# Optimization experiments

Hardware: AMD Instinct MI355X
Metric: run time of the kernel (lower is better)

The kernel has to match this reference:

```python
import jax, jax.numpy as jnp
import numpy as np

NUM_HEADS = 32
NUM_KV_HEADS = 8
HEAD_DIM = 128
SCALE = 0.08838834764831845  # 1/sqrt(HEAD_DIM)
SEQ_LEN = 2048
NEG_INF = -1e30


def setup_inputs() -> dict:
    key = jax.random.key(0)
    k1, k2, k3 = jax.random.split(key, 3)
    query = jax.random.normal(k1, (SEQ_LEN, NUM_HEADS * HEAD_DIM), dtype=jnp.float32)
    key_t = jax.random.normal(k2, (SEQ_LEN, NUM_KV_HEADS * HEAD_DIM), dtype=jnp.float32)
    value = jax.random.normal(k3, (SEQ_LEN, NUM_KV_HEADS * HEAD_DIM), dtype=jnp.float32)
    return {"query": query, "key": key_t, "value": value}


def reference(query, key, value):
    S = query.shape[0]
    n_rep = NUM_HEADS // NUM_KV_HEADS
    # GQA: group q heads by kv head instead of materializing repeated K/V.
    q = query.reshape(S, NUM_KV_HEADS, n_rep, HEAD_DIM)   # [S, G, R, D]
    k = key.reshape(S, NUM_KV_HEADS, HEAD_DIM)            # [S, G, D]
    v = value.reshape(S, NUM_KV_HEADS, HEAD_DIM)          # [S, G, D]
    # scores: [G, R, S(query), S(key)]
    scores = jnp.einsum('sgrd,tgd->grst', q, k) * jnp.float32(SCALE)
    # causal mask (prefill: seq_len > 1 -> is_causal=True)
    causal = jnp.arange(S)[:, None] >= jnp.arange(S)[None, :]  # [S, S]
    scores = jnp.where(causal, scores, NEG_INF)
    probs = jax.nn.softmax(scores, axis=-1)
    out = jnp.einsum('grst,tgd->sgrd', probs, v)          # [S, G, R, D]
    return out.reshape(S, NUM_HEADS * HEAD_DIM)
```

## Files before the change

### kernel.cpp

```cpp
#include <hip/hip_runtime.h>


#define SEQ    2048
#define NH     32
#define NKV    8
#define DHEAD  128
#define QROW   (NH * DHEAD)
#define KVROW  (NKV * DHEAD)
#define SCALE  0.08838834764831845f
#define LOG2E  1.4426950408889634f
#define BN     64
#define PSTR   136

typedef __attribute__((ext_vector_type(8))) short bf16x8;
typedef __attribute__((ext_vector_type(8))) unsigned short u16x8;
typedef __attribute__((ext_vector_type(16))) float f32x16;
typedef __attribute__((ext_vector_type(4))) unsigned int u32x4;

static __device__ __forceinline__ unsigned short f2bf(float f) {
  unsigned int u = __float_as_uint(f);
  return (unsigned short)((u + 0x7fffu + ((u >> 16) & 1u)) >> 16);
}

static __device__ __forceinline__ unsigned cvtpk_bf16(float lo, float hi) {
  unsigned r;
  asm("v_cvt_pk_bf16_f32 %0, %1, %2" : "=v"(r) : "v"(lo), "v"(hi));
  return r;
}

static __device__ __forceinline__ f32x16 zero16() {
  f32x16 z;
#pragma unroll
  for (int i = 0; i < 16; ++i) z[i] = 0.f;
  return z;
}

__global__ __launch_bounds__(256) void prep_frag_kernel(
    const float* __restrict__ K, const float* __restrict__ V,
    unsigned short* __restrict__ Kf, unsigned short* __restrict__ Vf) {
  __shared__ unsigned short Ks[64 * PSTR];
  __shared__ unsigned short Vs[64 * PSTR];
  const int tb  = blockIdx.x;
  const int g   = blockIdx.y;
  const int t0  = tb * 64;
  const int tid = threadIdx.x;
#pragma unroll
  for (int e = 0; e < 8; ++e) {
    int fi = e * 256 + tid;
    int r  = fi >> 5;
    int c4 = fi & 31;
    const float4 kv = *(const float4*)(K + (size_t)(t0 + r) * KVROW + g * DHEAD + c4 * 4);
    ushort4 kb4 = {f2bf(kv.x), f2bf(kv.y), f2bf(kv.z), f2bf(kv.w)};
    *(ushort4*)&Ks[r * PSTR + c4 * 4] = kb4;
    const float4 vv = *(const float4*)(V + (size_t)(t0 + r) * KVROW + g * DHEAD + c4 * 4);
    ushort4 vb4 = {f2bf(vv.x), f2bf(vv.y), f2bf(vv.z), f2bf(vv.w)};
    *(ushort4*)&Vs[r * PSTR + c4 * 4] = vb4;
  }
  __syncthreads();
  const size_t tbase = ((size_t)(g * 32 + tb)) << 13;
#pragma unroll
  for (int q = 0; q < 4; ++q) {
    int slot = tid * 4 + q;
    int fk   = slot >> 6;
    int lane = slot & 63;
    int l32v = lane & 31, hiv = lane >> 5;
    int row  = (fk >> 3) * 32 + l32v;
    int col  = (fk & 7) * 16 + hiv * 8;
    u16x8 o = *(const u16x8*)&Ks[row * PSTR + col];
    *(u16x8*)(Kf + tbase + slot * 8) = o;
  }
#pragma unroll
  for (int q = 0; q < 4; ++q) {
    int slot = tid * 4 + q;
    int fv   = slot >> 6;
    int lane = slot & 63;
    int l32v = lane & 31, hiv = lane >> 5;
    int d    = (fv & 3) * 32 + l32v;
    int key  = (fv >> 2) * 16 + hiv * 8;
    u16x8 o;
#pragma unroll
    for (int j = 0; j < 8; ++j) o[j] = Vs[(key + j) * PSTR + d];
    *(u16x8*)(Vf + tbase + slot * 8) = o;
  }
}

static __device__ __forceinline__ void load_qf(
    const float* __restrict__ Q, int q0, int h, int l32, int hi, bf16x8* qf) {
  const float* qp = Q + (size_t)(q0 + l32) * QROW + h * DHEAD + hi * 8;
#pragma unroll
  for (int ks = 0; ks < 8; ++ks) {
    const float4 a = *(const float4*)(qp + ks * 16);
    const float4 c = *(const float4*)(qp + ks * 16 + 4);
    bf16x8 v;
    v[0] = (short)f2bf(a.x * (SCALE * LOG2E));
    v[1] = (short)f2bf(a.y * (SCALE * LOG2E));
    v[2] = (short)f2bf(a.z * (SCALE * LOG2E));
    v[3] = (short)f2bf(a.w * (SCALE * LOG2E));
    v[4] = (short)f2bf(c.x * (SCALE * LOG2E));
    v[5] = (short)f2bf(c.y * (SCALE * LOG2E));
    v[6] = (short)f2bf(c.z * (SCALE * LOG2E));
    v[7] = (short)f2bf(c.w * (SCALE * LOG2E));
    qf[ks] = v;
  }
}

#define PV_KSTEP(PP, S, KS2)                                                     \
  do {                                                                           \
    unsigned y0 = cvtpk_bf16((PP)[(2 * (S)) * 4 + 0], (PP)[(2 * (S)) * 4 + 1]);  \
    unsigned z0 = cvtpk_bf16((PP)[(2 * (S)) * 4 + 2], (PP)[(2 * (S)) * 4 + 3]);  \
    unsigned y1 = cvtpk_bf16((PP)[(2 * (S) + 1) * 4 + 0], (PP)[(2 * (S) + 1) * 4 + 1]); \
    unsigned z1 = cvtpk_bf16((PP)[(2 * (S) + 1) * 4 + 2], (PP)[(2 * (S) + 1) * 4 + 3]); \
    asm("v_permlane32_swap_b32 %0, %1" : "+v"(y0), "+v"(y1));                    \
    asm("v_permlane32_swap_b32 %0, %1" : "+v"(z0), "+v"(z1));                    \
    u32x4 paw = (u32x4){y0, z0, y1, z1};                                         \
    bf16x8 pa = __builtin_bit_cast(bf16x8, paw);                                 \
    _Pragma("unroll")                                                            \
    for (int nd = 0; nd < 4; ++nd) {                                             \
      bf16x8 vf = *(const bf16x8*)(Vt + ((KS2) * 4 + nd) * 512 + lane * 8);      \
      oacc[nd] = __builtin_amdgcn_mfma_f32_32x32x16_bf16(pa, vf, oacc[nd], 0, 0, 0); \
    }                                                                            \
  } while (0)

static __device__ __forceinline__ void compute_tile_g(
    const unsigned short* __restrict__ Kt, const unsigned short* __restrict__ Vt,
    const bf16x8* qf, f32x16* oacc, float& lsum,
    int keyb, int q0, bool diag, int KB, int l32, int hi, int lane) {
  bf16x8 kf[8], kf2[8];
#pragma unroll
  for (int ks = 0; ks < 8; ++ks)
    kf[ks] = *(const bf16x8*)(Kt + ks * 512 + lane * 8);
  if (KB == 2) {
#pragma unroll
    for (int ks = 0; ks < 8; ++ks)
      kf2[ks] = *(const bf16x8*)(Kt + (8 + ks) * 512 + lane * 8);
  }
  f32x16 s0 = zero16();
  f32x16 s1 = zero16();
  __builtin_amdgcn_s_setprio(1);
#pragma unroll
  for (int ks = 0; ks < 8; ++ks)
    s0 = __builtin_amdgcn_mfma_f32_32x32x16_bf16(kf[ks], qf[ks], s0, 0, 0, 0);
  if (KB == 2) {
#pragma unroll
    for (int ks = 0; ks < 8; ++ks)
      s1 = __builtin_amdgcn_mfma_f32_32x32x16_bf16(kf2[ks], qf[ks], s1, 0, 0, 0);
  }
  __builtin_amdgcn_s_setprio(0);

  f32x16 p0, p1;
  if (!diag) {
#pragma unroll
    for (int r = 0; r < 16; ++r) { float e = __builtin_amdgcn_exp2f(s0[r]); p0[r] = e; lsum += e; }
#pragma unroll
    for (int r = 0; r < 16; ++r) { float e = __builtin_amdgcn_exp2f(s1[r]); p1[r] = e; lsum += e; }
  } else {
#pragma unroll
    for (int r = 0; r < 16; ++r) {
      const int ko = (r & 3) + 8 * (r >> 2) + 4 * hi;
      float x = (keyb + ko > q0 + l32) ? -1e30f : s0[r];
      float e = __builtin_amdgcn_exp2f(x);
      p0[r] = e; lsum += e;
    }
    if (KB == 2) {
#pragma unroll
      for (int r = 0; r < 16; ++r) {
        const int ko = 32 + (r & 3) + 8 * (r >> 2) + 4 * hi;
        float x = (keyb + ko > q0 + l32) ? -1e30f : s1[r];
        float e = __builtin_amdgcn_exp2f(x);
        p1[r] = e; lsum += e;
      }
    }
  }

  __builtin_amdgcn_s_setprio(1);
  PV_KSTEP(p0, 0, 0);
  PV_KSTEP(p0, 1, 1);
  if (KB == 2) {
    PV_KSTEP(p1, 0, 2);
    PV_KSTEP(p1, 1, 3);
  }
  __builtin_amdgcn_s_setprio(0);
}

__global__ __launch_bounds__(512, 2) void sdpa_frag_kernel(
    const float* __restrict__ Q, float* __restrict__ O,
    const unsigned short* __restrict__ Kf, const unsigned short* __restrict__ Vf) {
  __shared__ float Obuf[4][32 * 128];
  __shared__ float Lb[4][32];

  const int b    = blockIdx.x;
  const int g    = b & 7;
  const int p    = b >> 3;
  const int nt_l = (p + 2) >> 1;
  const int nt_h = 33 - nt_l;
  const int jj_h = 63 - p;
  const int jj_l = p;
  const int tid  = threadIdx.x;
  const int w    = tid >> 6;
  const int lane = tid & 63;
  const int l32  = lane & 31;
  const int hi   = lane >> 5;
  const int grp  = w >> 2;
  const int wg   = w & 3;
  const int h    = g * 4 + wg;

  int q0 = (grp ? jj_l : jj_h) * 32;

  bf16x8 qf[8];
  load_qf(Q, q0, h, l32, hi, qf);

  f32x16 oacc[4];
#pragma unroll
  for (int i = 0; i < 4; ++i) oacc[i] = zero16();
  float lsum = 0.f;

  const int niters = grp ? 16 : 17;
#pragma unroll 1
  for (int i = 0; i < niters; ++i) {
    int t, jjc;
    bool diag;
    if (grp == 0)      { t = i;                jjc = jj_h; diag = (nt_h == 17) && (i == 16); }
    else if (i < nt_l) { t = i;                jjc = jj_l; diag = (i == nt_l - 1); }
    else               { t = 17 + i - nt_l;    jjc = jj_h; diag = (i == 15); }
    const int KB = (diag && !(jjc & 1)) ? 1 : 2;
    const unsigned short* Kt = Kf + (((size_t)(g * 32 + t)) << 13);
    const unsigned short* Vt = Vf + (((size_t)(g * 32 + t)) << 13);
    compute_tile_g(Kt, Vt, qf, oacc, lsum, t * BN, q0, diag, KB, l32, hi, lane);

    if (grp == 1 && i == nt_l - 1) {
      float tot = lsum + __shfl_xor(lsum, 32);
      float inv = 1.f / tot;
#pragma unroll
      for (int nd = 0; nd < 4; ++nd)
#pragma unroll
        for (int r = 0; r < 16; ++r) {
          const int row = (r & 3) + 8 * (r >> 2) + 4 * hi;
          O[(size_t)(q0 + row) * QROW + h * DHEAD + nd * 32 + l32] =
              oacc[nd][r] * __shfl(inv, row);
        }
#pragma unroll
      for (int i2 = 0; i2 < 4; ++i2) oacc[i2] = zero16();
      lsum = 0.f;
      q0 = jj_h * 32;
      load_qf(Q, q0, h, l32, hi, qf);
    }
  }

  float tot = lsum + __shfl_xor(lsum, 32);
  if (grp == 1) {
    if (hi == 0) Lb[wg][l32] = tot;
    float* ob = &Obuf[wg][0];
#pragma unroll
    for (int nd = 0; nd < 4; ++nd)
#pragma unroll
      for (int r = 0; r < 16; ++r) {
        const int row = (r & 3) + 8 * (r >> 2) + 4 * hi;
        ob[row * 128 + nd * 32 + l32] = oacc[nd][r];
      }
  }
  __syncthreads();
  if (grp == 0) {
    tot += Lb[wg][l32];
    float inv = 1.f / tot;
    const float* ob = &Obuf[wg][0];
#pragma unroll
    for (int nd = 0; nd < 4; ++nd)
#pragma unroll
      for (int r = 0; r < 16; ++r) {
        const int row = (r & 3) + 8 * (r >> 2) + 4 * hi;
        float val = oacc[nd][r] + ob[row * 128 + nd * 32 + l32];
        O[(size_t)(q0 + row) * QROW + h * DHEAD + nd * 32 + l32] =
            val * __shfl(inv, row);
      }
  }
}

extern "C" void kernel_launch(void* const* d_in, const int* in_sizes, int n_in,
                              void* d_out, int out_size, void* d_ws, size_t ws_size,
                              hipStream_t stream) {
  (void)in_sizes; (void)n_in; (void)out_size; (void)ws_size;
  const float* Q = (const float*)d_in[0];
  const float* K = (const float*)d_in[1];
  const float* V = (const float*)d_in[2];
  float* O = (float*)d_out;
  unsigned short* Kf = (unsigned short*)d_ws;
  unsigned short* Vf = Kf + (size_t)NKV * SEQ * DHEAD;
  prep_frag_kernel<<<dim3(32, 8), 256, 0, stream>>>(K, V, Kf, Vf);
  sdpa_frag_kernel<<<256, 512, 0, stream>>>(Q, O, Kf, Vf);
}
```

Before: 152.6 us.

## Split each query tile's key range across four waves with LDS atomic reduction

Replaces the paired light/heavy query-tile scheme, where 8 waves in a block cover 4 heads across two query tiles, with one block per (kv group, head, query tile). The four waves in that block stride over the causal key tiles and combine partial outputs and row sums through shared-memory atomics before a vectorized normalized store. The grid grows from 256 to 2048 blocks to balance load through scheduling rather than manual pairing. The setprio hints are also removed. In exchange, K/V tiles are no longer shared across the 4 heads within a block, and the LDS atomic reduction adds cost.

```diff
diff --git a/kernel.cpp b/kernel.cpp
--- a/kernel.cpp
+++ b/kernel.cpp
@@ -136,7 +136,6 @@
   }
   f32x16 s0 = zero16();
   f32x16 s1 = zero16();
-  __builtin_amdgcn_s_setprio(1);
 #pragma unroll
   for (int ks = 0; ks < 8; ++ks)
     s0 = __builtin_amdgcn_mfma_f32_32x32x16_bf16(kf[ks], qf[ks], s0, 0, 0, 0);
@@ -145,7 +144,6 @@
     for (int ks = 0; ks < 8; ++ks)
       s1 = __builtin_amdgcn_mfma_f32_32x32x16_bf16(kf2[ks], qf[ks], s1, 0, 0, 0);
   }
-  __builtin_amdgcn_s_setprio(0);
 
   f32x16 p0, p1;
   if (!diag) {
@@ -172,39 +170,33 @@
     }
   }
 
-  __builtin_amdgcn_s_setprio(1);
   PV_KSTEP(p0, 0, 0);
   PV_KSTEP(p0, 1, 1);
   if (KB == 2) {
     PV_KSTEP(p1, 0, 2);
     PV_KSTEP(p1, 1, 3);
   }
-  __builtin_amdgcn_s_setprio(0);
-}
-
-__global__ __launch_bounds__(512, 2) void sdpa_frag_kernel(
+}
+
+__global__ __launch_bounds__(256, 4) void sdpa_split4_kernel(
     const float* __restrict__ Q, float* __restrict__ O,
     const unsigned short* __restrict__ Kf, const unsigned short* __restrict__ Vf) {
-  __shared__ float Obuf[4][32 * 128];
-  __shared__ float Lb[4][32];
-
-  const int b    = blockIdx.x;
-  const int g    = b & 7;
-  const int p    = b >> 3;
-  const int nt_l = (p + 2) >> 1;
-  const int nt_h = 33 - nt_l;
-  const int jj_h = 63 - p;
-  const int jj_l = p;
+  __shared__ float Obuf[32 * 128];
+  __shared__ float Lbuf[32];
+
+  const int b      = blockIdx.x;
+  const int g      = b & 7;
+  const int hh     = (b >> 3) & 3;
+  const int jjcode = b >> 5;
+  const int jj     = 63 - jjcode;
+  const int q0     = jj * 32;
+  const int nt     = (jj >> 1) + 1;
   const int tid  = threadIdx.x;
-  const int w    = tid >> 6;
+  const int s    = tid >> 6;
   const int lane = tid & 63;
   const int l32  = lane & 31;
   const int hi   = lane >> 5;
-  const int grp  = w >> 2;
-  const int wg   = w & 3;
-  const int h    = g * 4 + wg;
-
-  int q0 = (grp ? jj_l : jj_h) * 32;
+  const int h    = g * 4 + hh;
 
   bf16x8 qf[8];
   load_qf(Q, q0, h, l32, hi, qf);
@@ -214,64 +206,43 @@
   for (int i = 0; i < 4; ++i) oacc[i] = zero16();
   float lsum = 0.f;
 
-  const int niters = grp ? 16 : 17;
 #pragma unroll 1
-  for (int i = 0; i < niters; ++i) {
-    int t, jjc;
-    bool diag;
-    if (grp == 0)      { t = i;                jjc = jj_h; diag = (nt_h == 17) && (i == 16); }
-    else if (i < nt_l) { t = i;                jjc = jj_l; diag = (i == nt_l - 1); }
-    else               { t = 17 + i - nt_l;    jjc = jj_h; diag = (i == 15); }
-    const int KB = (diag && !(jjc & 1)) ? 1 : 2;
-    const unsigned short* Kt = Kf + (((size_t)(g * 32 + t)) << 13);
-    const unsigned short* Vt = Vf + (((size_t)(g * 32 + t)) << 13);
-    compute_tile_g(Kt, Vt, qf, oacc, lsum, t * BN, q0, diag, KB, l32, hi, lane);
-
-    if (grp == 1 && i == nt_l - 1) {
-      float tot = lsum + __shfl_xor(lsum, 32);
-      float inv = 1.f / tot;
-#pragma unroll
-      for (int nd = 0; nd < 4; ++nd)
-#pragma unroll
-        for (int r = 0; r < 16; ++r) {
-          const int row = (r & 3) + 8 * (r >> 2) + 4 * hi;
-          O[(size_t)(q0 + row) * QROW + h * DHEAD + nd * 32 + l32] =
-              oacc[nd][r] * __shfl(inv, row);
-        }
-#pragma unroll
-      for (int i2 = 0; i2 < 4; ++i2) oacc[i2] = zero16();
-      lsum = 0.f;
-      q0 = jj_h * 32;
-      load_qf(Q, q0, h, l32, hi, qf);
-    }
-  }
-
-  float tot = lsum + __shfl_xor(lsum, 32);
-  if (grp == 1) {
-    if (hi == 0) Lb[wg][l32] = tot;
-    float* ob = &Obuf[wg][0];
-#pragma unroll
-    for (int nd = 0; nd < 4; ++nd)
-#pragma unroll
-      for (int r = 0; r < 16; ++r) {
-        const int row = (r & 3) + 8 * (r >> 2) + 4 * hi;
-        ob[row * 128 + nd * 32 + l32] = oacc[nd][r];
-      }
-  }
+  for (int kt = s; kt < nt; kt += 4) {
+    const bool diag = (kt == nt - 1);
+    const int KB = (diag && !(jj & 1)) ? 1 : 2;
+    const unsigned short* Kt = Kf + (((size_t)(g * 32 + kt)) << 13);
+    const unsigned short* Vt = Vf + (((size_t)(g * 32 + kt)) << 13);
+    compute_tile_g(Kt, Vt, qf, oacc, lsum, kt * BN, q0, diag, KB, l32, hi, lane);
+  }
+
+  for (int i = tid; i < 32 * 128; i += 256) Obuf[i] = 0.f;
+  if (tid < 32) Lbuf[tid] = 0.f;
   __syncthreads();
-  if (grp == 0) {
-    tot += Lb[wg][l32];
-    float inv = 1.f / tot;
-    const float* ob = &Obuf[wg][0];
-#pragma unroll
-    for (int nd = 0; nd < 4; ++nd)
-#pragma unroll
-      for (int r = 0; r < 16; ++r) {
-        const int row = (r & 3) + 8 * (r >> 2) + 4 * hi;
-        float val = oacc[nd][r] + ob[row * 128 + nd * 32 + l32];
-        O[(size_t)(q0 + row) * QROW + h * DHEAD + nd * 32 + l32] =
-            val * __shfl(inv, row);
-      }
+  {
+    float tot = lsum + __shfl_xor(lsum, 32);
+    if (hi == 0) atomicAdd(&Lbuf[l32], tot);
+  }
+#pragma unroll
+  for (int nd = 0; nd < 4; ++nd)
+#pragma unroll
+    for (int r = 0; r < 16; ++r) {
+      const int row = (r & 3) + 8 * (r >> 2) + 4 * hi;
+      atomicAdd(&Obuf[row * 128 + nd * 32 + l32], oacc[nd][r]);
+    }
+  __syncthreads();
+
+  {
+    const int row = tid >> 3;
+    const int c0  = (tid & 7) * 16;
+    const float inv = 1.f / Lbuf[row];
+    float* orow = O + (size_t)(q0 + row) * QROW + h * DHEAD + c0;
+    const float* src = &Obuf[row * 128 + c0];
+#pragma unroll
+    for (int j = 0; j < 4; ++j) {
+      float4 v = *(const float4*)(src + j * 4);
+      v.x *= inv; v.y *= inv; v.z *= inv; v.w *= inv;
+      *(float4*)(orow + j * 4) = v;
+    }
   }
 }
 
@@ -286,5 +257,5 @@
   unsigned short* Kf = (unsigned short*)d_ws;
   unsigned short* Vf = Kf + (size_t)NKV * SEQ * DHEAD;
   prep_frag_kernel<<<dim3(32, 8), 256, 0, stream>>>(K, V, Kf, Vf);
-  sdpa_frag_kernel<<<256, 512, 0, stream>>>(Q, O, Kf, Vf);
-}
+  sdpa_split4_kernel<<<2048, 256, 0, stream>>>(Q, O, Kf, Vf);
+}
```

After: 420.9 us. 176% more time.
